# Performance work log

Measured on AMD Instinct MI355X. Metric: run time of the kernel, lower is better.

Reference implementation:

```python
import jax, jax.numpy as jnp
import numpy as np

B, N, H = 8, 2048, 256


def setup_inputs() -> dict:
    key = jax.random.key(0)
    ks = jax.random.split(key, 8)
    s = 1.0 / np.sqrt(H)
    return {
        "node": jax.random.normal(ks[0], (B, N, H), dtype=jnp.float32),
        "graph": jax.random.uniform(ks[1], (B, N, N), dtype=jnp.float32),
        "W1": jax.random.normal(ks[2], (H, H), dtype=jnp.float32) * s,
        "b1": jnp.zeros((H,), dtype=jnp.float32),
        "W2": jax.random.normal(ks[3], (H, H), dtype=jnp.float32) * s,
        "b2": jnp.zeros((H,), dtype=jnp.float32),
        "Wout": jax.random.normal(ks[4], (H, 2 * H), dtype=jnp.float32) * (1.0 / np.sqrt(2 * H)),
        "bout": jnp.zeros((H,), dtype=jnp.float32),
    }


def reference(node, graph, W1, b1, W2, b2, Wout, bout):
    # Symmetric normalization D^{-1/2} A D^{-1/2}, batched and vectorized
    # (equivalent to the per-sample diag-mm loop in the original).
    d = jnp.sum(graph, axis=2)                # [B, N] row sums (torch sum(1) on [N,N])
    dinv = d ** -0.5                          # [B, N]
    g = graph * dinv[:, :, None] * dinv[:, None, :]  # [B, N, N]

    # node_info = relu(fc1(g @ node)); fc2(g @ node_info)
    h = jax.nn.relu(jnp.einsum("bnm,bmh->bnh", g, node) @ W1.T + b1)
    h = jax.nn.relu(jnp.einsum("bnm,bmh->bnh", g, h) @ W2.T + b2)

    agg = jnp.concatenate([node, h], axis=2)  # [B, N, 2H]
    return jax.nn.relu(agg @ Wout.T + bout)   # [B, N, H]
```

## Files before the change

kernel.cpp:

```cpp
#include <hip/hip_runtime.h>
#include <stdint.h>

typedef __attribute__((ext_vector_type(4))) float f32x4;
typedef __attribute__((ext_vector_type(8))) short bf16x8;

static __device__ __forceinline__ unsigned short f2bf(float x) {
  unsigned int u = __builtin_bit_cast(unsigned int, x);
  u = (u + 0x7fffu + ((u >> 16) & 1u)) >> 16;
  return (unsigned short)u;
}

#define GLD16(g, l)                                                            \
  __builtin_amdgcn_global_load_lds(                                            \
      (__attribute__((address_space(1))) const void*)(g),                      \
      (__attribute__((address_space(3))) void*)(l), 16, 0, 0)

__global__ __launch_bounds__(256) void row_rsqrt_k(const float* __restrict__ g,
                                                   float* __restrict__ dinv) {
  int row = blockIdx.x * 4 + (threadIdx.x >> 6);
  int lane = threadIdx.x & 63;
  const float* p = g + (long)row * 2048;
  float s = 0.f;
#pragma unroll
  for (int i = 0; i < 8; ++i) {
    float4 v = *(const float4*)(p + (lane + i * 64) * 4);
    s += v.x + v.y + v.z + v.w;
  }
#pragma unroll
  for (int off = 32; off; off >>= 1) s += __shfl_xor(s, off, 64);
  if (lane == 0) dinv[row] = rsqrtf(s);
}

__global__ __launch_bounds__(256) void cvt_w_k(const float* __restrict__ W1,
                                               const float* __restrict__ W2,
                                               const float* __restrict__ Wout,
                                               unsigned short* __restrict__ wb) {
  int idx = blockIdx.x * 256 + threadIdx.x;
  float v;
  if (idx < 65536) v = W1[idx];
  else if (idx < 131072) v = W2[idx - 65536];
  else v = Wout[idx - 131072];
  wb[idx] = f2bf(v);
}

__global__ __launch_bounds__(256) void prep_node_k(
    const float* __restrict__ node, const float* __restrict__ dinv,
    unsigned short* __restrict__ nodeT, unsigned short* __restrict__ agg) {
  __shared__ unsigned short t[64 * 68];
  int tid = threadIdx.x;
  int m0 = blockIdx.x * 64, h0 = blockIdx.y * 64;
  long b = blockIdx.z;
#pragma unroll
  for (int i = 0; i < 4; ++i) {
    int idx = tid + 256 * i;
    int r = idx >> 4, c4 = idx & 15;
    long m = m0 + r;
    float4 v = *(const float4*)(node + (b * 2048 + m) * 256 + h0 + c4 * 4);
    float di = dinv[b * 2048 + m];
    ushort4 u;
    u.x = f2bf(v.x); u.y = f2bf(v.y); u.z = f2bf(v.z); u.w = f2bf(v.w);
    *(ushort4*)(agg + (b * 2048 + m) * 512 + h0 + c4 * 4) = u;
    t[(c4 * 4 + 0) * 68 + r] = f2bf(v.x * di);
    t[(c4 * 4 + 1) * 68 + r] = f2bf(v.y * di);
    t[(c4 * 4 + 2) * 68 + r] = f2bf(v.z * di);
    t[(c4 * 4 + 3) * 68 + r] = f2bf(v.w * di);
  }
  __syncthreads();
#pragma unroll
  for (int i = 0; i < 4; ++i) {
    int idx = tid + 256 * i;
    int hr = idx >> 4, c4 = idx & 15;
    ushort4 o = *(const ushort4*)(&t[hr * 68 + c4 * 4]);
    *(ushort4*)(nodeT + (b * 256 + h0 + hr) * 2048 + m0 + c4 * 4) = o;
  }
}

template <bool A_BF16, bool BIAS, bool RELU, bool SCALE, bool TRANS, bool OUTF32>
__global__ __launch_bounds__(256) void gemm_bt(
    const void* __restrict__ Ap, const unsigned short* __restrict__ Bt,
    const float* __restrict__ bias, const float* __restrict__ scale,
    void* __restrict__ Cp, int K, long aBatch, long btBatch, long cBatch,
    int lda, int ldbt, int ldc) {
  __shared__ char lds[81920];
  char* ldsA = lds;
  char* ldsB = lds + 16384;

  int tid = threadIdx.x;
  int lane = tid & 63;
  int w = tid >> 6;

  int fid = blockIdx.y * gridDim.x + blockIdx.x;
  int batch = fid & 7;
  int tile = fid >> 3;
  int bm0 = tile * 64;

  const float* Af32 = (const float*)Ap + (A_BF16 ? 0 : (long)batch * aBatch);
  const unsigned short* Abf =
      (const unsigned short*)Ap + (A_BF16 ? (long)batch * aBatch : 0);
  const unsigned short* Bb = Bt + (long)batch * btBatch;

  int nt = K >> 6;

  f32x4 acc[4][4] = {};
  float4 areg[4];

  auto stageB = [&](int kt, int buf) {
    char* base = ldsB + buf * 32768;
#pragma unroll
    for (int i = 0; i < 8; ++i) {
      int slot = (w * 8 + i) * 64 + lane;
      int c = slot >> 3, j = slot & 7;
      int jg = j ^ (c & 7);
      const unsigned short* src = Bb + (long)c * ldbt + kt * 64 + jg * 8;
      GLD16(src, base + (w * 8 + i) * 1024);
    }
  };
  auto stageA_lds = [&](int kt, int buf) {
    char* base = ldsA + buf * 8192;
#pragma unroll
    for (int i = 0; i < 2; ++i) {
      int slot = (w * 2 + i) * 64 + lane;
      int r = slot >> 3, j = slot & 7;
      int jg = j ^ (r & 7);
      const unsigned short* src = Abf + (long)(bm0 + r) * lda + kt * 64 + jg * 8;
      GLD16(src, base + (w * 2 + i) * 1024);
    }
  };
  auto loadA_regs = [&](int kt) {
#pragma unroll
    for (int i = 0; i < 4; ++i) {
      int idx = tid + 256 * i;
      int r = idx >> 4, c4 = idx & 15;
      areg[i] = *(const float4*)(Af32 + (long)(bm0 + r) * lda + kt * 64 + c4 * 4);
    }
  };
  auto writeA = [&](int buf) {
    char* base = ldsA + buf * 8192;
#pragma unroll
    for (int i = 0; i < 4; ++i) {
      int idx = tid + 256 * i;
      int r = idx >> 4, c4 = idx & 15;
      ushort4 h;
      h.x = f2bf(areg[i].x); h.y = f2bf(areg[i].y);
      h.z = f2bf(areg[i].z); h.w = f2bf(areg[i].w);
      int off = (r * 128 + c4 * 8) ^ ((r & 7) << 4);
      *(ushort4*)(base + off) = h;
    }
  };
  auto compute = [&](int buf) {
    char* bA = ldsA + buf * 8192;
    char* bB = ldsB + buf * 32768;
    bf16x8 a[4][2], bb[4][2];
#pragma unroll
    for (int m = 0; m < 4; ++m)
#pragma unroll
      for (int kk = 0; kk < 2; ++kk) {
        int row = m * 16 + (lane & 15);
        int off = (row * 128 + kk * 64 + (lane >> 4) * 16) ^ ((row & 7) << 4);
        a[m][kk] = *(const bf16x8*)(bA + off);
      }
#pragma unroll
    for (int n = 0; n < 4; ++n)
#pragma unroll
      for (int kk = 0; kk < 2; ++kk) {
        int col = w * 64 + n * 16 + (lane & 15);
        int off = (col * 128 + kk * 64 + (lane >> 4) * 16) ^ ((col & 7) << 4);
        bb[n][kk] = *(const bf16x8*)(bB + off);
      }
#pragma unroll
    for (int m = 0; m < 4; ++m)
#pragma unroll
      for (int n = 0; n < 4; ++n) {
        acc[m][n] = __builtin_amdgcn_mfma_f32_16x16x32_bf16(a[m][0], bb[n][0],
                                                            acc[m][n], 0, 0, 0);
        acc[m][n] = __builtin_amdgcn_mfma_f32_16x16x32_bf16(a[m][1], bb[n][1],
                                                            acc[m][n], 0, 0, 0);
      }
  };

  if (A_BF16) stageA_lds(0, 0);
  else { loadA_regs(0); writeA(0); }
  stageB(0, 0);
  __syncthreads();

  int cur = 0;
  for (int t = 0; t < nt; ++t) {
    int nxt = cur ^ 1;
    bool pf = (t + 1 < nt);
    if (pf) {
      if (A_BF16) stageA_lds(t + 1, nxt);
      else loadA_regs(t + 1);
      stageB(t + 1, nxt);
    }
    compute(cur);
    if (pf && !A_BF16) writeA(nxt);
    __syncthreads();
    cur = nxt;
  }

#pragma unroll
  for (int m = 0; m < 4; ++m) {
#pragma unroll
    for (int n = 0; n < 4; ++n) {
      int col = w * 64 + n * 16 + (lane & 15);
      float bv = BIAS ? bias[col] : 0.f;
#pragma unroll
      for (int r = 0; r < 4; ++r) {
        int row = m * 16 + (lane >> 4) * 4 + r;
        float v = acc[m][n][r];
        if (BIAS) v += bv;
        if (RELU) v = fmaxf(v, 0.f);
        if (SCALE) v *= scale[(long)batch * 2048 + bm0 + row];
        if (OUTF32) {
          float* C = (float*)Cp + (long)batch * cBatch;
          C[(long)(bm0 + row) * ldc + col] = v;
        } else {
          unsigned short* C = (unsigned short*)Cp + (long)batch * cBatch;
          if (TRANS) C[(long)col * ldc + (bm0 + row)] = f2bf(v);
          else C[(long)(bm0 + row) * ldc + col] = f2bf(v);
        }
      }
    }
  }
}

extern "C" void kernel_launch(void* const* d_in, const int* in_sizes, int n_in,
                              void* d_out, int out_size, void* d_ws,
                              size_t ws_size, hipStream_t stream) {
  const float* node = (const float*)d_in[0];
  const float* graph = (const float*)d_in[1];
  const float* W1 = (const float*)d_in[2];
  const float* b1 = (const float*)d_in[3];
  const float* W2 = (const float*)d_in[4];
  const float* b2 = (const float*)d_in[5];
  const float* Wout = (const float*)d_in[6];
  const float* bout = (const float*)d_in[7];
  float* out = (float*)d_out;

  char* p = (char*)d_ws;
  float* dinv = (float*)p;              p += 16384 * 4;
  unsigned short* wb = (unsigned short*)p; p += 262144 * 2;
  unsigned short* nodeT = (unsigned short*)p; p += 8L * 256 * 2048 * 2;
  unsigned short* bufT = (unsigned short*)p;  p += 8L * 2048 * 256 * 2;
  unsigned short* agg = (unsigned short*)p;   p += 8L * 2048 * 512 * 2;

  row_rsqrt_k<<<4096, 256, 0, stream>>>(graph, dinv);
  cvt_w_k<<<1024, 256, 0, stream>>>(W1, W2, Wout, wb);
  prep_node_k<<<dim3(32, 4, 8), 256, 0, stream>>>(node, dinv, nodeT, agg);

  gemm_bt<false, false, false, true, false, false>
      <<<dim3(32, 8), 256, 0, stream>>>(graph, nodeT, nullptr, dinv, bufT, 2048,
                                        2048L * 2048, 256L * 2048, 2048L * 256,
                                        2048, 2048, 256);
  gemm_bt<true, true, true, true, true, false>
      <<<dim3(32, 8), 256, 0, stream>>>(bufT, wb, b1, dinv, nodeT, 256,
                                        2048L * 256, 0, 256L * 2048,
                                        256, 256, 2048);
  gemm_bt<false, false, false, true, false, false>
      <<<dim3(32, 8), 256, 0, stream>>>(graph, nodeT, nullptr, dinv, bufT, 2048,
                                        2048L * 2048, 256L * 2048, 2048L * 256,
                                        2048, 2048, 256);
  gemm_bt<true, true, true, false, false, false>
      <<<dim3(32, 8), 256, 0, stream>>>(bufT, wb + 65536, b2, nullptr, agg + 256,
                                        256, 2048L * 256, 0, 2048L * 512,
                                        256, 256, 512);
  gemm_bt<true, true, true, false, false, true>
      <<<dim3(32, 8), 256, 0, stream>>>(agg, wb + 131072, bout, nullptr, out,
                                        512, 2048L * 512, 0, 2048L * 256,
                                        512, 512, 256);
}
```

Baseline: 333.9 us.

## Pre-convert row-scaled graph to bf16 and use 32-row GEMM tiles

The row-sum kernel now also writes the graph, scaled by its row D^-1/2, as bf16 into a workspace buffer. Both graph GEMMs then stream bf16 through direct global-to-LDS loads instead of reading fp32 and converting in registers, and the row scale no longer needs an epilogue multiply. The GEMM tile shrinks to 32 rows with a flat 512-block grid to raise parallelism, and the transposed epilogue stages through LDS so stores are coalesced. The cost is an extra 64MB bf16 write, and each B tile (nodeT or weights) is re-read by twice as many blocks.

```diff
diff --git a/kernel.cpp b/kernel.cpp
--- a/kernel.cpp
+++ b/kernel.cpp
@@ -15,20 +15,31 @@
       (__attribute__((address_space(1))) const void*)(g),                      \
       (__attribute__((address_space(3))) void*)(l), 16, 0, 0)
 
-__global__ __launch_bounds__(256) void row_rsqrt_k(const float* __restrict__ g,
-                                                   float* __restrict__ dinv) {
+__global__ __launch_bounds__(256) void rowscale_cvt_k(
+    const float* __restrict__ g, float* __restrict__ dinv,
+    unsigned short* __restrict__ gb) {
   int row = blockIdx.x * 4 + (threadIdx.x >> 6);
   int lane = threadIdx.x & 63;
   const float* p = g + (long)row * 2048;
+  float4 v[8];
   float s = 0.f;
 #pragma unroll
   for (int i = 0; i < 8; ++i) {
-    float4 v = *(const float4*)(p + (lane + i * 64) * 4);
-    s += v.x + v.y + v.z + v.w;
+    v[i] = *(const float4*)(p + (lane + i * 64) * 4);
+    s += v[i].x + v[i].y + v[i].z + v[i].w;
   }
 #pragma unroll
   for (int off = 32; off; off >>= 1) s += __shfl_xor(s, off, 64);
-  if (lane == 0) dinv[row] = rsqrtf(s);
+  float di = rsqrtf(s);
+  if (lane == 0) dinv[row] = di;
+  unsigned short* q = gb + (long)row * 2048;
+#pragma unroll
+  for (int i = 0; i < 8; ++i) {
+    ushort4 u;
+    u.x = f2bf(v[i].x * di); u.y = f2bf(v[i].y * di);
+    u.z = f2bf(v[i].z * di); u.w = f2bf(v[i].w * di);
+    *(ushort4*)(q + (lane + i * 64) * 4) = u;
+  }
 }
 
 __global__ __launch_bounds__(256) void cvt_w_k(const float* __restrict__ W1,
@@ -75,35 +86,35 @@
   }
 }
 
-template <bool A_BF16, bool BIAS, bool RELU, bool SCALE, bool TRANS, bool OUTF32>
-__global__ __launch_bounds__(256) void gemm_bt(
-    const void* __restrict__ Ap, const unsigned short* __restrict__ Bt,
+template <bool BIAS, bool RELU, bool SCALE, bool TRANS, bool OUTF32>
+__global__ __launch_bounds__(256) void gemm32(
+    const unsigned short* __restrict__ A, const unsigned short* __restrict__ Bt,
     const float* __restrict__ bias, const float* __restrict__ scale,
-    void* __restrict__ Cp, int K, long aBatch, long btBatch, long cBatch,
-    int lda, int ldbt, int ldc) {
-  __shared__ char lds[81920];
+    void* __restrict__ Cp, int K, int lda, int ldbt, long bBatch, int ldc) {
+  __shared__ char lds[73728];
   char* ldsA = lds;
-  char* ldsB = lds + 16384;
+  char* ldsB = lds + 8192;
 
   int tid = threadIdx.x;
   int lane = tid & 63;
   int w = tid >> 6;
 
-  int fid = blockIdx.y * gridDim.x + blockIdx.x;
-  int batch = fid & 7;
-  int tile = fid >> 3;
-  int bm0 = tile * 64;
-
-  const float* Af32 = (const float*)Ap + (A_BF16 ? 0 : (long)batch * aBatch);
-  const unsigned short* Abf =
-      (const unsigned short*)Ap + (A_BF16 ? (long)batch * aBatch : 0);
-  const unsigned short* Bb = Bt + (long)batch * btBatch;
+  int bid = blockIdx.x;
+  int tile = ((bid & 7) << 6) + (bid >> 3);
+  int row0 = tile * 32;
+  int batch = row0 >> 11;
+  const unsigned short* Bb = Bt + (long)batch * bBatch;
 
   int nt = K >> 6;
-
-  f32x4 acc[4][4] = {};
-  float4 areg[4];
-
+  f32x4 acc[2][4] = {};
+
+  auto stageA = [&](int kt, int buf) {
+    int slot = w * 64 + lane;
+    int r = slot >> 3, j = slot & 7;
+    int jg = j ^ (r & 7);
+    GLD16(A + (long)(row0 + r) * lda + kt * 64 + jg * 8,
+          ldsA + buf * 4096 + w * 1024);
+  };
   auto stageB = [&](int kt, int buf) {
     char* base = ldsB + buf * 32768;
 #pragma unroll
@@ -111,48 +122,15 @@
       int slot = (w * 8 + i) * 64 + lane;
       int c = slot >> 3, j = slot & 7;
       int jg = j ^ (c & 7);
-      const unsigned short* src = Bb + (long)c * ldbt + kt * 64 + jg * 8;
-      GLD16(src, base + (w * 8 + i) * 1024);
-    }
-  };
-  auto stageA_lds = [&](int kt, int buf) {
-    char* base = ldsA + buf * 8192;
-#pragma unroll
-    for (int i = 0; i < 2; ++i) {
-      int slot = (w * 2 + i) * 64 + lane;
-      int r = slot >> 3, j = slot & 7;
-      int jg = j ^ (r & 7);
-      const unsigned short* src = Abf + (long)(bm0 + r) * lda + kt * 64 + jg * 8;
-      GLD16(src, base + (w * 2 + i) * 1024);
-    }
-  };
-  auto loadA_regs = [&](int kt) {
-#pragma unroll
-    for (int i = 0; i < 4; ++i) {
-      int idx = tid + 256 * i;
-      int r = idx >> 4, c4 = idx & 15;
-      areg[i] = *(const float4*)(Af32 + (long)(bm0 + r) * lda + kt * 64 + c4 * 4);
-    }
-  };
-  auto writeA = [&](int buf) {
-    char* base = ldsA + buf * 8192;
-#pragma unroll
-    for (int i = 0; i < 4; ++i) {
-      int idx = tid + 256 * i;
-      int r = idx >> 4, c4 = idx & 15;
-      ushort4 h;
-      h.x = f2bf(areg[i].x); h.y = f2bf(areg[i].y);
-      h.z = f2bf(areg[i].z); h.w = f2bf(areg[i].w);
-      int off = (r * 128 + c4 * 8) ^ ((r & 7) << 4);
-      *(ushort4*)(base + off) = h;
+      GLD16(Bb + (long)c * ldbt + kt * 64 + jg * 8, base + (w * 8 + i) * 1024);
     }
   };
   auto compute = [&](int buf) {
-    char* bA = ldsA + buf * 8192;
+    char* bA = ldsA + buf * 4096;
     char* bB = ldsB + buf * 32768;
-    bf16x8 a[4][2], bb[4][2];
-#pragma unroll
-    for (int m = 0; m < 4; ++m)
+    bf16x8 a[2][2], bb[4][2];
+#pragma unroll
+    for (int m = 0; m < 2; ++m)
 #pragma unroll
       for (int kk = 0; kk < 2; ++kk) {
         int row = m * 16 + (lane & 15);
@@ -168,7 +146,7 @@
         bb[n][kk] = *(const bf16x8*)(bB + off);
       }
 #pragma unroll
-    for (int m = 0; m < 4; ++m)
+    for (int m = 0; m < 2; ++m)
 #pragma unroll
       for (int n = 0; n < 4; ++n) {
         acc[m][n] = __builtin_amdgcn_mfma_f32_16x16x32_bf16(a[m][0], bb[n][0],
@@ -178,49 +156,68 @@
       }
   };
 
-  if (A_BF16) stageA_lds(0, 0);
-  else { loadA_regs(0); writeA(0); }
+  stageA(0, 0);
   stageB(0, 0);
   __syncthreads();
 
   int cur = 0;
   for (int t = 0; t < nt; ++t) {
     int nxt = cur ^ 1;
-    bool pf = (t + 1 < nt);
-    if (pf) {
-      if (A_BF16) stageA_lds(t + 1, nxt);
-      else loadA_regs(t + 1);
+    if (t + 1 < nt) {
+      stageA(t + 1, nxt);
       stageB(t + 1, nxt);
     }
     compute(cur);
-    if (pf && !A_BF16) writeA(nxt);
     __syncthreads();
     cur = nxt;
   }
 
-#pragma unroll
-  for (int m = 0; m < 4; ++m) {
-#pragma unroll
-    for (int n = 0; n < 4; ++n) {
-      int col = w * 64 + n * 16 + (lane & 15);
-      float bv = BIAS ? bias[col] : 0.f;
-#pragma unroll
-      for (int r = 0; r < 4; ++r) {
-        int row = m * 16 + (lane >> 4) * 4 + r;
-        float v = acc[m][n][r];
-        if (BIAS) v += bv;
-        if (RELU) v = fmaxf(v, 0.f);
-        if (SCALE) v *= scale[(long)batch * 2048 + bm0 + row];
-        if (OUTF32) {
-          float* C = (float*)Cp + (long)batch * cBatch;
-          C[(long)(bm0 + row) * ldc + col] = v;
-        } else {
-          unsigned short* C = (unsigned short*)Cp + (long)batch * cBatch;
-          if (TRANS) C[(long)col * ldc + (bm0 + row)] = f2bf(v);
-          else C[(long)(bm0 + row) * ldc + col] = f2bf(v);
+  if (TRANS) {
+    unsigned short* tb = (unsigned short*)lds;
+#pragma unroll
+    for (int m = 0; m < 2; ++m)
+#pragma unroll
+      for (int n = 0; n < 4; ++n) {
+        int col = w * 64 + n * 16 + (lane & 15);
+        float bv = BIAS ? bias[col] : 0.f;
+#pragma unroll
+        for (int r = 0; r < 4; ++r) {
+          int rl = m * 16 + (lane >> 4) * 4 + r;
+          float v = acc[m][n][r];
+          if (BIAS) v += bv;
+          if (RELU) v = fmaxf(v, 0.f);
+          if (SCALE) v *= scale[row0 + rl];
+          tb[col * 40 + rl] = f2bf(v);
         }
       }
+    __syncthreads();
+    unsigned short* C = (unsigned short*)Cp;
+    int rin = row0 & 2047;
+#pragma unroll
+    for (int cc = 0; cc < 4; ++cc) {
+      int col = (tid >> 2) + cc * 64;
+      int seg = tid & 3;
+      bf16x8 u = *(const bf16x8*)(tb + col * 40 + seg * 8);
+      *(bf16x8*)(C + ((long)batch * 256 + col) * 2048 + rin + seg * 8) = u;
     }
+  } else {
+#pragma unroll
+    for (int m = 0; m < 2; ++m)
+#pragma unroll
+      for (int n = 0; n < 4; ++n) {
+        int col = w * 64 + n * 16 + (lane & 15);
+        float bv = BIAS ? bias[col] : 0.f;
+#pragma unroll
+        for (int r = 0; r < 4; ++r) {
+          long row = row0 + m * 16 + (lane >> 4) * 4 + r;
+          float v = acc[m][n][r];
+          if (BIAS) v += bv;
+          if (RELU) v = fmaxf(v, 0.f);
+          if (SCALE) v *= scale[row];
+          if (OUTF32) ((float*)Cp)[row * ldc + col] = v;
+          else ((unsigned short*)Cp)[row * ldc + col] = f2bf(v);
+        }
+      }
   }
 }
 
@@ -238,34 +235,25 @@
   float* out = (float*)d_out;
 
   char* p = (char*)d_ws;
-  float* dinv = (float*)p;              p += 16384 * 4;
-  unsigned short* wb = (unsigned short*)p; p += 262144 * 2;
+  float* dinv = (float*)p;                    p += 16384 * 4;
+  unsigned short* wb = (unsigned short*)p;    p += 262144 * 2;
+  unsigned short* gb = (unsigned short*)p;    p += 8L * 2048 * 2048 * 2;
   unsigned short* nodeT = (unsigned short*)p; p += 8L * 256 * 2048 * 2;
   unsigned short* bufT = (unsigned short*)p;  p += 8L * 2048 * 256 * 2;
   unsigned short* agg = (unsigned short*)p;   p += 8L * 2048 * 512 * 2;
 
-  row_rsqrt_k<<<4096, 256, 0, stream>>>(graph, dinv);
+  rowscale_cvt_k<<<4096, 256, 0, stream>>>(graph, dinv, gb);
   cvt_w_k<<<1024, 256, 0, stream>>>(W1, W2, Wout, wb);
   prep_node_k<<<dim3(32, 4, 8), 256, 0, stream>>>(node, dinv, nodeT, agg);
 
-  gemm_bt<false, false, false, true, false, false>
-      <<<dim3(32, 8), 256, 0, stream>>>(graph, nodeT, nullptr, dinv, bufT, 2048,
-                                        2048L * 2048, 256L * 2048, 2048L * 256,
-                                        2048, 2048, 256);
-  gemm_bt<true, true, true, true, true, false>
-      <<<dim3(32, 8), 256, 0, stream>>>(bufT, wb, b1, dinv, nodeT, 256,
-                                        2048L * 256, 0, 256L * 2048,
-                                        256, 256, 2048);
-  gemm_bt<false, false, false, true, false, false>
-      <<<dim3(32, 8), 256, 0, stream>>>(graph, nodeT, nullptr, dinv, bufT, 2048,
-                                        2048L * 2048, 256L * 2048, 2048L * 256,
-                                        2048, 2048, 256);
-  gemm_bt<true, true, true, false, false, false>
-      <<<dim3(32, 8), 256, 0, stream>>>(bufT, wb + 65536, b2, nullptr, agg + 256,
-                                        256, 2048L * 256, 0, 2048L * 512,
-                                        256, 256, 512);
-  gemm_bt<true, true, true, false, false, true>
-      <<<dim3(32, 8), 256, 0, stream>>>(agg, wb + 131072, bout, nullptr, out,
-                                        512, 2048L * 512, 0, 2048L * 256,
-                                        512, 512, 256);
-}
+  gemm32<false, false, false, false, false><<<512, 256, 0, stream>>>(
+      gb, nodeT, nullptr, nullptr, bufT, 2048, 2048, 2048, 256L * 2048, 256);
+  gemm32<true, true, true, true, false><<<512, 256, 0, stream>>>(
+      bufT, wb, b1, dinv, nodeT, 256, 256, 256, 0, 2048);
+  gemm32<false, false, false, false, false><<<512, 256, 0, stream>>>(
+      gb, nodeT, nullptr, nullptr, bufT, 2048, 2048, 2048, 256L * 2048, 256);
+  gemm32<true, true, false, false, false><<<512, 256, 0, stream>>>(
+      bufT, wb + 65536, b2, nullptr, agg + 256, 256, 256, 256, 0, 512);
+  gemm32<true, true, false, false, true><<<512, 256, 0, stream>>>(
+      agg, wb + 131072, bout, nullptr, out, 512, 512, 512, 0, 256);
+}
```

Result: faster. 314.0 us (-5.9%).
